# Kernel optimization log

Measured on AMD Instinct MI355X. Metric: run time of the kernel, lower is better.

## Reference

```python
import jax, jax.numpy as jnp
import numpy as np

N = 100000

def _gcn_norm(edge_index, n):
    # PyG GCNConv default: add self-loops, symmetric deg^-1/2 normalization
    loops = jnp.arange(n, dtype=edge_index.dtype)
    src = jnp.concatenate([edge_index[0], loops])
    dst = jnp.concatenate([edge_index[1], loops])
    deg = jax.ops.segment_sum(jnp.ones_like(dst, dtype=jnp.float32), dst, num_segments=n)
    dinv = jnp.where(deg > 0, jax.lax.rsqrt(deg), 0.0)
    norm = dinv[src] * dinv[dst]  # [E+N]
    return src, dst, norm

def _gcn_conv(h, W, b, src, dst, norm, n):
    # transform then gather-scale-scatter aggregate
    h = h @ W                                   # [N, out]
    out = jax.ops.segment_sum(norm[:, None] * h[src], dst, num_segments=n)
    return out + b

def _prelu(h, a):
    return jnp.where(h > 0, h, a * h)

def _dropout(h, u, p=0.5):
    # deterministic dropout: keep where u >= p, scale by 1/(1-p)
    return jnp.where(u >= p, h / (1.0 - p), 0.0)

def setup_inputs() -> dict:
    key = jax.random.key(0)
    ks = jax.random.split(key, 12)
    D, H1, H2, C, E = 512, 128, 16, 10, 1600000
    x = jax.random.normal(ks[0], (N, D), dtype=jnp.float32)
    edge_index = jax.random.randint(ks[1], (2, E), 0, N, dtype=jnp.int64)
    u1 = jax.random.uniform(ks[2], (N, H1), dtype=jnp.float32)
    u2 = jax.random.uniform(ks[3], (N, H2), dtype=jnp.float32)
    def glorot(k, shp):
        lim = np.sqrt(6.0 / (shp[0] + shp[1]))
        return jax.random.uniform(k, shp, dtype=jnp.float32, minval=-lim, maxval=lim)
    W1 = glorot(ks[4], (D, H1)); b1 = jnp.zeros((H1,), jnp.float32)
    W2 = glorot(ks[5], (H1, H2)); b2 = jnp.zeros((H2,), jnp.float32)
    fcW = glorot(ks[6], (H2, C)); fcb = jnp.zeros((C,), jnp.float32)
    a = jnp.float32(0.25)  # PReLU init (shared single param for both layers)
    return {"x": x, "edge_index": edge_index, "W1": W1, "b1": b1, "W2": W2,
            "b2": b2, "a": a, "fcW": fcW, "fcb": fcb, "u1": u1, "u2": u2}

def reference(x, edge_index, W1, b1, W2, b2, a, fcW, fcb, u1, u2):
    src, dst, norm = _gcn_norm(edge_index, N)
    feat1 = _dropout(_prelu(_gcn_conv(x, W1, b1, src, dst, norm, N), a), u1)
    feat2 = _dropout(_prelu(_gcn_conv(feat1, W2, b2, src, dst, norm, N), a), u2)
    logits = feat2 @ fcW + fcb
    return (feat2, logits)
```

## Files before the change

kernel.cpp:

```cpp
#include <hip/hip_runtime.h>
#include <hip/hip_bf16.h>
#include <stdint.h>

#define NN 100000
#define DIN 512
#define H1C 128
#define H2C 16
#define NCLS 10
#define NB_SCAN ((NN + 255) / 256)

typedef __attribute__((ext_vector_type(8))) short s16x8;
typedef __attribute__((ext_vector_type(4))) float f32x4;
typedef __attribute__((ext_vector_type(4))) unsigned short u16x4;
typedef __attribute__((ext_vector_type(8))) unsigned short u16x8;

static __device__ __forceinline__ unsigned short f2bf(float f) {
  __hip_bfloat16 h = __float2bfloat16(f);
  return *(unsigned short*)&h;
}
static __device__ __forceinline__ float bflo(unsigned u) {
  return __uint_as_float(u << 16);
}
static __device__ __forceinline__ float bfhi(unsigned u) {
  return __uint_as_float(u & 0xffff0000u);
}

__global__ void k_detect(const int* __restrict__ ei, int* __restrict__ flag) {
  int lane = threadIdx.x;
  int v = ei[2 * lane + 1];
  unsigned long long b = __ballot(v == 0);
  if (lane == 0) *flag = (b == ~0ull) ? 1 : 0;
}

__device__ __forceinline__ int ld_src(const int* __restrict__ ei, int f, int E, int i) {
  return f ? ei[2 * (size_t)i] : ei[i];
}
__device__ __forceinline__ int ld_dst(const int* __restrict__ ei, int f, int E, int i) {
  return f ? ei[2 * ((size_t)E + (size_t)i)] : ei[(size_t)E + (size_t)i];
}

__global__ void k_initdeg(int* __restrict__ deg, int n) {
  int i = blockIdx.x * blockDim.x + threadIdx.x;
  if (i < n) deg[i] = 0;
}

__global__ void k_count(const int* __restrict__ ei, const int* __restrict__ flag,
                        int E, int* __restrict__ deg, int* __restrict__ rank) {
  int i = blockIdx.x * blockDim.x + threadIdx.x;
  if (i >= E) return;
  int f = *flag;
  rank[i] = atomicAdd(&deg[ld_dst(ei, f, E, i)], 1);
}

__global__ void k_dinv(const int* __restrict__ deg, float* __restrict__ dinv, int n) {
  int i = blockIdx.x * blockDim.x + threadIdx.x;
  if (i < n) dinv[i] = rsqrtf((float)(deg[i] + 1));
}

__global__ void k_scanA(const int* __restrict__ deg, int* __restrict__ incl,
                        int* __restrict__ bsum, int n) {
  __shared__ int s[256];
  int i = blockIdx.x * 256 + threadIdx.x;
  int v = (i < n) ? deg[i] : 0;
  s[threadIdx.x] = v;
  __syncthreads();
  for (int off = 1; off < 256; off <<= 1) {
    int t = (threadIdx.x >= off) ? s[threadIdx.x - off] : 0;
    __syncthreads();
    s[threadIdx.x] += t;
    __syncthreads();
  }
  if (i < n) incl[i] = s[threadIdx.x];
  if (threadIdx.x == 255) bsum[blockIdx.x] = s[255];
}

__global__ void k_scanB(int* __restrict__ bsum, int nb) {
  __shared__ int s[512];
  int v = (threadIdx.x < nb) ? bsum[threadIdx.x] : 0;
  s[threadIdx.x] = v;
  __syncthreads();
  for (int off = 1; off < 512; off <<= 1) {
    int t = (threadIdx.x >= off) ? s[threadIdx.x - off] : 0;
    __syncthreads();
    s[threadIdx.x] += t;
    __syncthreads();
  }
  if (threadIdx.x < nb) bsum[threadIdx.x] = s[threadIdx.x] - v;
}

__global__ void k_scanC(const int* __restrict__ deg, const int* __restrict__ bsum,
                        int* __restrict__ offs, int n, int E) {
  int i = blockIdx.x * 256 + threadIdx.x;
  if (i < n) offs[i] = offs[i] - deg[i] + bsum[i >> 8];
  if (i == 0) offs[n] = E;
}

__global__ void k_scatter(const int* __restrict__ ei, const int* __restrict__ flag, int E,
                          const int* __restrict__ offs, const int* __restrict__ rank,
                          const float* __restrict__ dinv, uint2* __restrict__ csr_sw) {
  int i = blockIdx.x * blockDim.x + threadIdx.x;
  if (i >= E) return;
  int f = *flag;
  int s = ld_src(ei, f, E, i), d = ld_dst(ei, f, E, i);
  int pos = offs[d] + rank[i];
  uint2 rec;
  rec.x = (unsigned)s;
  rec.y = __float_as_uint(dinv[s]);
  csr_sw[pos] = rec;
}

__global__ void k_wt(const float* __restrict__ W1, unsigned short* __restrict__ Wt) {
  int t = blockIdx.x * 256 + threadIdx.x;
  int nn = t >> 9, k = t & 511;
  Wt[t] = f2bf(W1[(size_t)k * H1C + nn]);
}

#define BM 64
#define BK 64
#define LDA 72
#define LDB 72

__global__ __launch_bounds__(256) void k_gemm1_mfma(const float* __restrict__ x,
                                                    const unsigned short* __restrict__ Wt,
                                                    unsigned int* __restrict__ h1u, int n) {
  __shared__ unsigned short As[BM * LDA];
  __shared__ unsigned short Bs[H1C * LDB];
  int tid = threadIdx.x;
  int wave = tid >> 6, lane = tid & 63;
  int wm = wave >> 1, wn = wave & 1;
  int bm = blockIdx.x * BM;
  int lrow = lane & 15, lk = (lane >> 4) * 8;

  f32x4 acc[2][4];
#pragma unroll
  for (int i = 0; i < 2; i++)
#pragma unroll
    for (int j = 0; j < 4; j++) acc[i][j] = (f32x4){0.f, 0.f, 0.f, 0.f};

  for (int k0 = 0; k0 < DIN; k0 += BK) {
#pragma unroll
    for (int p = 0; p < 4; p++) {
      int idx = p * 256 + tid;
      int r = idx >> 4, c4 = (idx & 15) * 4;
      int row = bm + r;
      float4 v = make_float4(0.f, 0.f, 0.f, 0.f);
      if (row < n) v = *(const float4*)(x + (size_t)row * DIN + k0 + c4);
      u16x4 b4;
      b4.x = f2bf(v.x); b4.y = f2bf(v.y); b4.z = f2bf(v.z); b4.w = f2bf(v.w);
      *(u16x4*)&As[r * LDA + c4] = b4;
    }
#pragma unroll
    for (int p = 0; p < 4; p++) {
      int idx = p * 256 + tid;
      int r = idx >> 3, c8 = (idx & 7) * 8;
      int pr = (r & 64) + (((r & 1) + 2 * ((r >> 5) & 1)) << 4) + ((r >> 1) & 15);
      u16x8 v = *(const u16x8*)&Wt[(size_t)r * DIN + k0 + c8];
      *(u16x8*)&Bs[pr * LDB + c8] = v;
    }
    __syncthreads();
#pragma unroll
    for (int kk = 0; kk < 2; kk++) {
      s16x8 a[2], b[4];
#pragma unroll
      for (int mi = 0; mi < 2; mi++)
        a[mi] = *(const s16x8*)&As[(wm * 32 + mi * 16 + lrow) * LDA + kk * 32 + lk];
#pragma unroll
      for (int nj = 0; nj < 4; nj++)
        b[nj] = *(const s16x8*)&Bs[(wn * 64 + nj * 16 + lrow) * LDB + kk * 32 + lk];
#pragma unroll
      for (int mi = 0; mi < 2; mi++)
#pragma unroll
        for (int nj = 0; nj < 4; nj++)
          acc[mi][nj] = __builtin_amdgcn_mfma_f32_16x16x32_bf16(a[mi], b[nj], acc[mi][nj], 0, 0, 0);
    }
    __syncthreads();
  }
#pragma unroll
  for (int mi = 0; mi < 2; mi++) {
#pragma unroll
    for (int r = 0; r < 4; r++) {
      int row = bm + wm * 32 + mi * 16 + (lane >> 4) * 4 + r;
      if (row < n) {
        unsigned p0 = ((unsigned)f2bf(acc[mi][1][r]) << 16) | (unsigned)f2bf(acc[mi][0][r]);
        unsigned p1 = ((unsigned)f2bf(acc[mi][3][r]) << 16) | (unsigned)f2bf(acc[mi][2][r]);
        h1u[(size_t)row * 64 + wn * 32 + lrow] = p0;
        h1u[(size_t)row * 64 + wn * 32 + 16 + lrow] = p1;
      }
    }
  }
}

__global__ __launch_bounds__(256) void k_agg1(const unsigned int* __restrict__ h1u,
                                              const uint2* __restrict__ csr_sw,
                                              const int* __restrict__ offs,
                                              const float* __restrict__ dinv,
                                              const float* __restrict__ b1,
                                              const float* __restrict__ aP,
                                              const float* __restrict__ u1,
                                              unsigned int* __restrict__ f1u, int n) {
  int wid = (blockIdx.x * 256 + threadIdx.x) >> 6;
  int lane = threadIdx.x & 63;
  if (wid >= n) return;
  int d = wid;
  int beg = offs[d], end = offs[d + 1];
  unsigned gs = h1u[(size_t)d * 64 + lane];
  float ax = 0.f, ay = 0.f;
  int e = beg;
  for (; e + 7 < end; e += 8) {
    uint2 r0 = csr_sw[e],     r1 = csr_sw[e + 1], r2 = csr_sw[e + 2], r3 = csr_sw[e + 3];
    uint2 r4 = csr_sw[e + 4], r5 = csr_sw[e + 5], r6 = csr_sw[e + 6], r7 = csr_sw[e + 7];
    unsigned g0 = h1u[(size_t)r0.x * 64 + lane];
    unsigned g1 = h1u[(size_t)r1.x * 64 + lane];
    unsigned g2 = h1u[(size_t)r2.x * 64 + lane];
    unsigned g3 = h1u[(size_t)r3.x * 64 + lane];
    unsigned g4 = h1u[(size_t)r4.x * 64 + lane];
    unsigned g5 = h1u[(size_t)r5.x * 64 + lane];
    unsigned g6 = h1u[(size_t)r6.x * 64 + lane];
    unsigned g7 = h1u[(size_t)r7.x * 64 + lane];
    float w0 = __uint_as_float(r0.y), w1 = __uint_as_float(r1.y);
    float w2 = __uint_as_float(r2.y), w3 = __uint_as_float(r3.y);
    float w4 = __uint_as_float(r4.y), w5 = __uint_as_float(r5.y);
    float w6 = __uint_as_float(r6.y), w7 = __uint_as_float(r7.y);
    ax += w0 * bflo(g0); ay += w0 * bfhi(g0);
    ax += w1 * bflo(g1); ay += w1 * bfhi(g1);
    ax += w2 * bflo(g2); ay += w2 * bfhi(g2);
    ax += w3 * bflo(g3); ay += w3 * bfhi(g3);
    ax += w4 * bflo(g4); ay += w4 * bfhi(g4);
    ax += w5 * bflo(g5); ay += w5 * bfhi(g5);
    ax += w6 * bflo(g6); ay += w6 * bfhi(g6);
    ax += w7 * bflo(g7); ay += w7 * bfhi(g7);
  }
  for (; e + 3 < end; e += 4) {
    uint2 r0 = csr_sw[e], r1 = csr_sw[e + 1], r2 = csr_sw[e + 2], r3 = csr_sw[e + 3];
    unsigned g0 = h1u[(size_t)r0.x * 64 + lane];
    unsigned g1 = h1u[(size_t)r1.x * 64 + lane];
    unsigned g2 = h1u[(size_t)r2.x * 64 + lane];
    unsigned g3 = h1u[(size_t)r3.x * 64 + lane];
    float w0 = __uint_as_float(r0.y), w1 = __uint_as_float(r1.y);
    float w2 = __uint_as_float(r2.y), w3 = __uint_as_float(r3.y);
    ax += w0 * bflo(g0); ay += w0 * bfhi(g0);
    ax += w1 * bflo(g1); ay += w1 * bfhi(g1);
    ax += w2 * bflo(g2); ay += w2 * bfhi(g2);
    ax += w3 * bflo(g3); ay += w3 * bfhi(g3);
  }
  for (; e < end; e++) {
    uint2 rr = csr_sw[e];
    float w = __uint_as_float(rr.y);
    unsigned g = h1u[(size_t)rr.x * 64 + lane];
    ax += w * bflo(g); ay += w * bfhi(g);
  }
  float di = dinv[d];
  ax = (ax + di * bflo(gs)) * di;
  ay = (ay + di * bfhi(gs)) * di;
  float2 bb = ((const float2*)b1)[lane];
  ax += bb.x; ay += bb.y;
  float al = *aP;
  ax = ax > 0.f ? ax : al * ax;
  ay = ay > 0.f ? ay : al * ay;
  float2 uu = ((const float2*)u1)[(size_t)d * 64 + lane];
  ax = (uu.x >= 0.5f) ? ax * 2.f : 0.f;
  ay = (uu.y >= 0.5f) ? ay * 2.f : 0.f;
  unsigned pk = ((unsigned)f2bf(ay) << 16) | (unsigned)f2bf(ax);
  f1u[(size_t)d * 64 + lane] = pk;
}

__global__ __launch_bounds__(256) void k_gemm2(const unsigned int* __restrict__ f1u,
                                               const float* __restrict__ W2,
                                               unsigned int* __restrict__ h2u, int n) {
  __shared__ float ws[H1C][H2C];
  __shared__ unsigned int fs[16][66];
  int tid = threadIdx.x;
#pragma unroll
  for (int p = 0; p < 8; p++) {
    int idx = tid + p * 256;
    ws[idx >> 4][idx & 15] = W2[idx];
  }
  int r0 = blockIdx.x * 16;
  {
    int r = tid >> 4, c4 = (tid & 15) * 4;
    int row = r0 + r;
    uint4 v = make_uint4(0, 0, 0, 0);
    if (row < n) v = *(const uint4*)(f1u + (size_t)row * 64 + c4);
    *(uint4*)&fs[r][c4] = v;
  }
  __syncthreads();
  int col = tid & 15, r = tid >> 4;
  float acc = 0.f;
#pragma unroll
  for (int k = 0; k < 64; k++) {
    unsigned u = fs[r][k];
    acc += bflo(u) * ws[2 * k][col] + bfhi(u) * ws[2 * k + 1][col];
  }
  int row = r0 + r;
  float accN = __shfl_xor(acc, 1, 64);
  if ((col & 1) == 0 && row < n) {
    unsigned pk = ((unsigned)f2bf(accN) << 16) | (unsigned)f2bf(acc);
    h2u[(size_t)row * 8 + (col >> 1)] = pk;
  }
}

__global__ __launch_bounds__(256) void k_agg2(const unsigned int* __restrict__ h2u,
                                              const uint2* __restrict__ csr_sw,
                                              const int* __restrict__ offs,
                                              const float* __restrict__ dinv,
                                              const float* __restrict__ b2,
                                              const float* __restrict__ aP,
                                              const float* __restrict__ u2,
                                              const float* __restrict__ fcW,
                                              const float* __restrict__ fcb,
                                              float* __restrict__ out_feat2,
                                              float* __restrict__ out_logits, int n) {
  int wid = (blockIdx.x * 256 + threadIdx.x) >> 6;
  int lane = threadIdx.x & 63;
  if (wid >= n) return;
  int d = wid;
  int g = lane >> 3, j = lane & 7;
  int beg = offs[d], end = offs[d + 1];
  unsigned gs = h2u[(size_t)d * 8 + j];
  float aa = 0.f, ab = 0.f;
  int e = beg + g;
  for (; e + 8 < end; e += 16) {
    uint2 r0 = csr_sw[e], r1 = csr_sw[e + 8];
    unsigned g0 = h2u[(size_t)r0.x * 8 + j];
    unsigned g1 = h2u[(size_t)r1.x * 8 + j];
    float w0 = __uint_as_float(r0.y), w1 = __uint_as_float(r1.y);
    aa += w0 * bflo(g0) + w1 * bflo(g1);
    ab += w0 * bfhi(g0) + w1 * bfhi(g1);
  }
  for (; e < end; e += 8) {
    uint2 rr = csr_sw[e];
    unsigned gg = h2u[(size_t)rr.x * 8 + j];
    float w = __uint_as_float(rr.y);
    aa += w * bflo(gg); ab += w * bfhi(gg);
  }
  aa += __shfl_xor(aa, 8, 64); aa += __shfl_xor(aa, 16, 64); aa += __shfl_xor(aa, 32, 64);
  ab += __shfl_xor(ab, 8, 64); ab += __shfl_xor(ab, 16, 64); ab += __shfl_xor(ab, 32, 64);
  float di = dinv[d];
  aa = (aa + di * bflo(gs)) * di;
  ab = (ab + di * bfhi(gs)) * di;
  aa += b2[2 * j]; ab += b2[2 * j + 1];
  float al = *aP;
  aa = aa > 0.f ? aa : al * aa;
  ab = ab > 0.f ? ab : al * ab;
  float2 uu = ((const float2*)(u2 + (size_t)d * H2C))[j];
  aa = (uu.x >= 0.5f) ? aa * 2.f : 0.f;
  ab = (uu.y >= 0.5f) ? ab * 2.f : 0.f;
  if (lane < 8) {
    float2 o; o.x = aa; o.y = ab;
    ((float2*)(out_feat2 + (size_t)d * H2C))[j] = o;
  }
  int c = lane & 15;
  int cc = (c < NCLS) ? c : 0;
  float lg = fcb[cc];
#pragma unroll
  for (int k = 0; k < 8; k++) {
    float va = __shfl(aa, k, 64);
    float vb = __shfl(ab, k, 64);
    lg += va * fcW[(2 * k) * NCLS + cc] + vb * fcW[(2 * k + 1) * NCLS + cc];
  }
  if (lane < NCLS) out_logits[(size_t)d * NCLS + c] = lg;
}

extern "C" void kernel_launch(void* const* d_in, const int* in_sizes, int n_in,
                              void* d_out, int out_size, void* d_ws, size_t ws_size,
                              hipStream_t stream) {
  const float* x   = (const float*)d_in[0];
  const int*   ei  = (const int*)d_in[1];
  const float* W1  = (const float*)d_in[2];
  const float* b1  = (const float*)d_in[3];
  const float* W2  = (const float*)d_in[4];
  const float* b2  = (const float*)d_in[5];
  const float* aP  = (const float*)d_in[6];
  const float* fcW = (const float*)d_in[7];
  const float* fcb = (const float*)d_in[8];
  const float* u1  = (const float*)d_in[9];
  const float* u2  = (const float*)d_in[10];
  const int E = in_sizes[1] / 2;

  float* out_feat2  = (float*)d_out;
  float* out_logits = (float*)d_out + (size_t)NN * H2C;

  char* w = (char*)d_ws;
  size_t off = 0;
  auto A = [&](size_t bytes) -> char* {
    char* p = w + off;
    off = (off + bytes + 255) & ~(size_t)255;
    return p;
  };
  int*   flag   = (int*)A(256);
  int*   deg    = (int*)A((size_t)NN * 4);
  int*   offs   = (int*)A((size_t)(NN + 1) * 4);
  float* dinv   = (float*)A((size_t)NN * 4);
  int*   bsum   = (int*)A(512 * 4);
  int*   rank   = (int*)A((size_t)E * 4);
  uint2* csr_sw = (uint2*)A((size_t)E * 8);
  unsigned int* h1u = (unsigned int*)A((size_t)NN * 64 * 4);
  unsigned int* f1u = (unsigned int*)A((size_t)NN * 64 * 4);
  unsigned int* h2u = (unsigned int*)A((size_t)NN * 8 * 4);
  unsigned short* Wt = (unsigned short*)A((size_t)H1C * DIN * 2);

  dim3 b256(256);
  int gE = (E + 255) / 256;
  int gN = (NN + 255) / 256;

  k_detect<<<1, 64, 0, stream>>>(ei, flag);
  k_initdeg<<<gN, b256, 0, stream>>>(deg, NN);
  k_count<<<gE, b256, 0, stream>>>(ei, flag, E, deg, rank);
  k_dinv<<<gN, b256, 0, stream>>>(deg, dinv, NN);
  k_scanA<<<NB_SCAN, b256, 0, stream>>>(deg, offs, bsum, NN);
  k_scanB<<<1, 512, 0, stream>>>(bsum, NB_SCAN);
  k_scanC<<<gN, b256, 0, stream>>>(deg, bsum, offs, NN, E);
  k_scatter<<<gE, b256, 0, stream>>>(ei, flag, E, offs, rank, dinv, csr_sw);
  k_wt<<<(H1C * DIN) / 256, b256, 0, stream>>>(W1, Wt);
  k_gemm1_mfma<<<(NN + BM - 1) / BM, b256, 0, stream>>>(x, Wt, h1u, NN);
  k_agg1<<<(NN + 3) / 4, b256, 0, stream>>>(h1u, csr_sw, offs, dinv, b1, aP, u1, f1u, NN);
  k_gemm2<<<(NN + 15) / 16, b256, 0, stream>>>(f1u, W2, h2u, NN);
  k_agg2<<<(NN + 3) / 4, b256, 0, stream>>>(h2u, csr_sw, offs, dinv, b2, aP, u2,
                                            fcW, fcb, out_feat2, out_logits, NN);
}
```

Measured before the change: 345.3 us.

## Fuse preprocessing kernels and double GEMM1 row tile to 128

Measured after the change: 370.7 us. 1.07x slower.

```diff
diff --git a/kernel.cpp b/kernel.cpp
--- a/kernel.cpp
+++ b/kernel.cpp
@@ -25,13 +25,6 @@
   return __uint_as_float(u & 0xffff0000u);
 }
 
-__global__ void k_detect(const int* __restrict__ ei, int* __restrict__ flag) {
-  int lane = threadIdx.x;
-  int v = ei[2 * lane + 1];
-  unsigned long long b = __ballot(v == 0);
-  if (lane == 0) *flag = (b == ~0ull) ? 1 : 0;
-}
-
 __device__ __forceinline__ int ld_src(const int* __restrict__ ei, int f, int E, int i) {
   return f ? ei[2 * (size_t)i] : ei[i];
 }
@@ -39,9 +32,20 @@
   return f ? ei[2 * ((size_t)E + (size_t)i)] : ei[(size_t)E + (size_t)i];
 }
 
-__global__ void k_initdeg(int* __restrict__ deg, int n) {
-  int i = blockIdx.x * blockDim.x + threadIdx.x;
+__global__ void k_pre(const int* __restrict__ ei, int* __restrict__ flag,
+                      int* __restrict__ deg,
+                      const float* __restrict__ W1, unsigned short* __restrict__ Wt, int n) {
+  int i = blockIdx.x * 256 + threadIdx.x;
+  if (blockIdx.x == 0 && threadIdx.x < 64) {
+    int v = ei[2 * threadIdx.x + 1];
+    unsigned long long b = __ballot(v == 0);
+    if (threadIdx.x == 0) *flag = (b == ~0ull) ? 1 : 0;
+  }
   if (i < n) deg[i] = 0;
+  if (i < H1C * DIN) {
+    int nn = i >> 9, k = i & 511;
+    Wt[i] = f2bf(W1[(size_t)k * H1C + nn]);
+  }
 }
 
 __global__ void k_count(const int* __restrict__ ei, const int* __restrict__ flag,
@@ -52,16 +56,12 @@
   rank[i] = atomicAdd(&deg[ld_dst(ei, f, E, i)], 1);
 }
 
-__global__ void k_dinv(const int* __restrict__ deg, float* __restrict__ dinv, int n) {
-  int i = blockIdx.x * blockDim.x + threadIdx.x;
-  if (i < n) dinv[i] = rsqrtf((float)(deg[i] + 1));
-}
-
 __global__ void k_scanA(const int* __restrict__ deg, int* __restrict__ incl,
-                        int* __restrict__ bsum, int n) {
+                        int* __restrict__ bsum, float* __restrict__ dinv, int n) {
   __shared__ int s[256];
   int i = blockIdx.x * 256 + threadIdx.x;
   int v = (i < n) ? deg[i] : 0;
+  if (i < n) dinv[i] = rsqrtf((float)(v + 1));
   s[threadIdx.x] = v;
   __syncthreads();
   for (int off = 1; off < 256; off <<= 1) {
@@ -109,13 +109,7 @@
   csr_sw[pos] = rec;
 }
 
-__global__ void k_wt(const float* __restrict__ W1, unsigned short* __restrict__ Wt) {
-  int t = blockIdx.x * 256 + threadIdx.x;
-  int nn = t >> 9, k = t & 511;
-  Wt[t] = f2bf(W1[(size_t)k * H1C + nn]);
-}
-
-#define BM 64
+#define BM 128
 #define BK 64
 #define LDA 72
 #define LDB 72
@@ -131,15 +125,15 @@
   int bm = blockIdx.x * BM;
   int lrow = lane & 15, lk = (lane >> 4) * 8;
 
-  f32x4 acc[2][4];
-#pragma unroll
-  for (int i = 0; i < 2; i++)
+  f32x4 acc[4][4];
+#pragma unroll
+  for (int i = 0; i < 4; i++)
 #pragma unroll
     for (int j = 0; j < 4; j++) acc[i][j] = (f32x4){0.f, 0.f, 0.f, 0.f};
 
   for (int k0 = 0; k0 < DIN; k0 += BK) {
 #pragma unroll
-    for (int p = 0; p < 4; p++) {
+    for (int p = 0; p < 8; p++) {
       int idx = p * 256 + tid;
       int r = idx >> 4, c4 = (idx & 15) * 4;
       int row = bm + r;
@@ -160,15 +154,15 @@
     __syncthreads();
 #pragma unroll
     for (int kk = 0; kk < 2; kk++) {
-      s16x8 a[2], b[4];
-#pragma unroll
-      for (int mi = 0; mi < 2; mi++)
-        a[mi] = *(const s16x8*)&As[(wm * 32 + mi * 16 + lrow) * LDA + kk * 32 + lk];
+      s16x8 a[4], b[4];
+#pragma unroll
+      for (int mi = 0; mi < 4; mi++)
+        a[mi] = *(const s16x8*)&As[(wm * 64 + mi * 16 + lrow) * LDA + kk * 32 + lk];
 #pragma unroll
       for (int nj = 0; nj < 4; nj++)
         b[nj] = *(const s16x8*)&Bs[(wn * 64 + nj * 16 + lrow) * LDB + kk * 32 + lk];
 #pragma unroll
-      for (int mi = 0; mi < 2; mi++)
+      for (int mi = 0; mi < 4; mi++)
 #pragma unroll
         for (int nj = 0; nj < 4; nj++)
           acc[mi][nj] = __builtin_amdgcn_mfma_f32_16x16x32_bf16(a[mi], b[nj], acc[mi][nj], 0, 0, 0);
@@ -176,10 +170,10 @@
     __syncthreads();
   }
 #pragma unroll
-  for (int mi = 0; mi < 2; mi++) {
+  for (int mi = 0; mi < 4; mi++) {
 #pragma unroll
     for (int r = 0; r < 4; r++) {
-      int row = bm + wm * 32 + mi * 16 + (lane >> 4) * 4 + r;
+      int row = bm + wm * 64 + mi * 16 + (lane >> 4) * 4 + r;
       if (row < n) {
         unsigned p0 = ((unsigned)f2bf(acc[mi][1][r]) << 16) | (unsigned)f2bf(acc[mi][0][r]);
         unsigned p1 = ((unsigned)f2bf(acc[mi][3][r]) << 16) | (unsigned)f2bf(acc[mi][2][r]);
@@ -403,15 +397,12 @@
   int gE = (E + 255) / 256;
   int gN = (NN + 255) / 256;
 
-  k_detect<<<1, 64, 0, stream>>>(ei, flag);
-  k_initdeg<<<gN, b256, 0, stream>>>(deg, NN);
+  k_pre<<<gN, b256, 0, stream>>>(ei, flag, deg, W1, Wt, NN);
   k_count<<<gE, b256, 0, stream>>>(ei, flag, E, deg, rank);
-  k_dinv<<<gN, b256, 0, stream>>>(deg, dinv, NN);
-  k_scanA<<<NB_SCAN, b256, 0, stream>>>(deg, offs, bsum, NN);
+  k_scanA<<<NB_SCAN, b256, 0, stream>>>(deg, offs, bsum, dinv, NN);
   k_scanB<<<1, 512, 0, stream>>>(bsum, NB_SCAN);
   k_scanC<<<gN, b256, 0, stream>>>(deg, bsum, offs, NN, E);
   k_scatter<<<gE, b256, 0, stream>>>(ei, flag, E, offs, rank, dinv, csr_sw);
-  k_wt<<<(H1C * DIN) / 256, b256, 0, stream>>>(W1, Wt);
   k_gemm1_mfma<<<(NN + BM - 1) / BM, b256, 0, stream>>>(x, Wt, h1u, NN);
   k_agg1<<<(NN + 3) / 4, b256, 0, stream>>>(h1u, csr_sw, offs, dinv, b1, aP, u1, f1u, NN);
   k_gemm2<<<(NN + 15) / 16, b256, 0, stream>>>(f1u, W2, h2u, NN);
```
